# Optimization experiments

Hardware: AMD Instinct MI355X
Metric: run time of the kernel (lower is better)

## Reference

```python
import jax, jax.numpy as jnp
import numpy as np

T, B, N, DEG, F_IN, H, C = 48, 32, 96, 8, 16, 128, 500
E = B * N * DEG          # edges per timestep (already batch-offset within [0, B*N))
M = T * B * N            # total nodes across all timesteps
EPS = 1e-5               # BatchNorm eps


def setup_inputs() -> dict:
    key = jax.random.key(0)
    ks = jax.random.split(key, 24)
    rn = lambda k, s: jax.random.normal(k, s, dtype=jnp.float32) * 0.05
    return {
        "x": jax.random.normal(ks[0], (T, B * N, F_IN), dtype=jnp.float32),
        "edge_index": jax.random.randint(ks[1], (T, 2, E), 0, B * N, dtype=jnp.int32),
        "gcn_w0": rn(ks[2], (F_IN, H)),
        "gcn_w12": rn(ks[3], (2, H, H)),
        "gcn_b": rn(ks[4], (3, H)),
        "bn_gamma": jnp.ones((3, H), dtype=jnp.float32),
        "bn_beta": jnp.zeros((3, H), dtype=jnp.float32),
        "bn_mean": rn(ks[5], (3, H)),
        "bn_var": jax.random.uniform(ks[6], (3, H), minval=0.5, maxval=1.5, dtype=jnp.float32),
        "lstm_wih0": rn(ks[7], (2, 4 * H, H)),
        "lstm_whh0": rn(ks[8], (2, 4 * H, H)),
        "lstm_bih0": rn(ks[9], (2, 4 * H)),
        "lstm_bhh0": rn(ks[10], (2, 4 * H)),
        "lstm_wih1": rn(ks[11], (2, 4 * H, 2 * H)),
        "lstm_whh1": rn(ks[12], (2, 4 * H, H)),
        "lstm_bih1": rn(ks[13], (2, 4 * H)),
        "lstm_bhh1": rn(ks[14], (2, 4 * H)),
        "attn_w1": rn(ks[15], (2 * H, H)),
        "attn_b1": rn(ks[16], (H,)),
        "attn_w2": rn(ks[17], (H, 1)),
        "attn_b2": rn(ks[18], (1,)),
        "fc1_w": rn(ks[19], (2 * H, H)),
        "fc1_b": rn(ks[20], (H,)),
        "fc2_w": rn(ks[21], (H, C)),
        "fc2_b": rn(ks[22], (C,)),
    }


def _lstm_dir(x, wih, whh, bih, bhh):
    # x: [T, B, I]; PyTorch gate order i, f, g, o
    pre = jnp.einsum('tbi,gi->tbg', x, wih) + bih  # input projection hoisted out of scan
    h0 = jnp.zeros((x.shape[1], whh.shape[1]), x.dtype)

    def step(carry, p):
        h, c = carry
        g = p + h @ whh.T + bhh
        i, f, gg, o = jnp.split(g, 4, axis=-1)
        c = jax.nn.sigmoid(f) * c + jax.nn.sigmoid(i) * jnp.tanh(gg)
        h = jax.nn.sigmoid(o) * jnp.tanh(c)
        return (h, c), h

    _, hs = jax.lax.scan(step, (h0, h0), pre)
    return hs  # [T, B, Hh]


def _bilstm(x, wih, whh, bih, bhh):
    fwd = _lstm_dir(x, wih[0], whh[0], bih[0], bhh[0])
    bwd = _lstm_dir(x[::-1], wih[1], whh[1], bih[1], bhh[1])[::-1]
    return jnp.concatenate([fwd, bwd], axis=-1)  # [T, B, 2H]


def reference(x, edge_index, gcn_w0, gcn_w12, gcn_b,
              bn_gamma, bn_beta, bn_mean, bn_var,
              lstm_wih0, lstm_whh0, lstm_bih0, lstm_bhh0,
              lstm_wih1, lstm_whh1, lstm_bih1, lstm_bhh1,
              attn_w1, attn_b1, attn_w2, attn_b2,
              fc1_w, fc1_b, fc2_w, fc2_b):
    # Fold timesteps into one big node set by offsetting indices by t*B*N
    off = (jnp.arange(T, dtype=jnp.int32) * (B * N))[:, None]
    src = (edge_index[:, 0] + off).reshape(-1)
    dst = (edge_index[:, 1] + off).reshape(-1)

    # GCN symmetric norm with self-loops: deg counts incoming edges + self-loop
    deg = jax.ops.segment_sum(jnp.ones_like(src, dtype=x.dtype), dst, num_segments=M) + 1.0
    dinv = jax.lax.rsqrt(deg)
    enorm = (dinv[src] * dinv[dst])[:, None]   # per-edge norm
    self_norm = (1.0 / deg)[:, None]           # self-loop norm

    h = x.reshape(M, F_IN)
    for l in range(3):
        W = gcn_w0 if l == 0 else gcn_w12[l - 1]
        hw = h @ W  # GCNConv applies linear first
        z = jax.ops.segment_sum(hw[src] * enorm, dst, num_segments=M) + hw * self_norm + gcn_b[l]
        # BatchNorm1d eval-mode (running stats), then ReLU, residual if shapes match
        z = (z - bn_mean[l]) * (bn_gamma[l] * jax.lax.rsqrt(bn_var[l] + EPS)) + bn_beta[l]
        z = jax.nn.relu(z)
        h = z + h if l > 0 else z  # dropout is identity in eval

    # global_mean_pool per graph (fixed N nodes per graph)
    emb = h.reshape(T, B, N, H).mean(axis=2)  # [T, B, H]

    out1 = _bilstm(emb, lstm_wih0, lstm_whh0, lstm_bih0, lstm_bhh0)
    out2 = _bilstm(out1, lstm_wih1, lstm_whh1, lstm_bih1, lstm_bhh1)
    lstm_out = out2.transpose(1, 0, 2)  # [B, T, 2H]

    a = jnp.tanh(lstm_out @ attn_w1 + attn_b1) @ attn_w2 + attn_b2  # [B, T, 1]
    w = jax.nn.softmax(a, axis=1)
    ws = jnp.sum(lstm_out * w, axis=1)  # [B, 2H]

    y = jax.nn.relu(ws @ fc1_w + fc1_b) @ fc2_w + fc2_b
    return jax.nn.log_softmax(y, axis=1)
```

## Files before the change

kernel.cpp:

```cpp
#include <hip/hip_runtime.h>

#define T_ 48
#define B_ 32
#define N_ 96
#define E_ 24576
#define BN_ (B_*N_)
#define M_ (T_*BN_)
#define FIN_ 16
#define H_ 128
#define C_ 500
#define TE_ (T_*E_)
#define EPS_ 1e-5f

typedef _Float16 f16x8 __attribute__((ext_vector_type(8)));
typedef float    f32x4 __attribute__((ext_vector_type(4)));
typedef _Float16 half2v __attribute__((ext_vector_type(2)));

__device__ __forceinline__ ushort f2h(float f) {
    _Float16 h = (_Float16)f;
    union { _Float16 h; ushort u; } v;
    v.h = h;
    return v.u;
}
__device__ __forceinline__ float h2f(ushort u) {
    union { ushort u; _Float16 h; } v;
    v.u = u;
    return (float)v.h;
}
__device__ __forceinline__ half2v pkfma(unsigned int v, unsigned int w, half2v acc) {
#if __has_builtin(__builtin_elementwise_fma)
    return __builtin_elementwise_fma(__builtin_bit_cast(half2v, v),
                                     __builtin_bit_cast(half2v, w), acc);
#else
    half2v hv = __builtin_bit_cast(half2v, v);
    half2v wv = __builtin_bit_cast(half2v, w);
    acc[0] += hv[0]*wv[0];
    acc[1] += hv[1]*wv[1];
    return acc;
#endif
}
__device__ __forceinline__ float dot2pk(unsigned int hbits, unsigned int wbits, float acc) {
#if __has_builtin(__builtin_amdgcn_fdot2)
    return __builtin_amdgcn_fdot2(__builtin_bit_cast(half2v, hbits),
                                  __builtin_bit_cast(half2v, wbits), acc, false);
#else
    half2v hv = __builtin_bit_cast(half2v, hbits);
    half2v wv = __builtin_bit_cast(half2v, wbits);
    acc = fmaf((float)hv[0], (float)wv[0], acc);
    acc = fmaf((float)hv[1], (float)wv[1], acc);
    return acc;
#endif
}
__device__ __forceinline__ float sigm(float x) {
    return 1.f / (1.f + __expf(-x));
}
__device__ __forceinline__ float ftanh(float x) {
    x = fminf(15.f, fmaxf(-15.f, x));
    float e = __expf(2.f * x);
    return (e - 1.f) / (e + 1.f);
}

__global__ __launch_bounds__(1024) void csr_build_k(
    const int* __restrict__ ei, int* __restrict__ csr_off,
    unsigned int* __restrict__ csr_pk, float* __restrict__ dinv)
{
    int t = blockIdx.x;
    int tid = threadIdx.x;
    __shared__ int cnt[BN_];
    __shared__ int cur[BN_];
    __shared__ int scanbuf[1024];
    __shared__ unsigned int pk[E_];

    #pragma unroll
    for (int i = 0; i < 3; i++) cnt[tid + i*1024] = 0;
    __syncthreads();

    const int* srcp = ei + ((long)t*2+0)*E_;
    const int* dstp = ei + ((long)t*2+1)*E_;
    #pragma unroll
    for (int i = 0; i < E_/1024; i++)
        atomicAdd(&cnt[dstp[tid + i*1024]], 1);
    __syncthreads();

    int n0 = tid*3;
    int a = cnt[n0], b = cnt[n0+1], c = cnt[n0+2];
    int tot = a + b + c;
    scanbuf[tid] = tot;
    __syncthreads();
    for (int d = 1; d < 1024; d <<= 1) {
        int add = (tid >= d) ? scanbuf[tid-d] : 0;
        __syncthreads();
        scanbuf[tid] += add;
        __syncthreads();
    }
    int excl = scanbuf[tid] - tot;
    cur[n0] = excl; cur[n0+1] = excl + a; cur[n0+2] = excl + a + b;
    int gbase = t*BN_, ebase = t*E_;
    csr_off[gbase+n0]   = ebase + excl;
    csr_off[gbase+n0+1] = ebase + excl + a;
    csr_off[gbase+n0+2] = ebase + excl + a + b;
    dinv[gbase+n0]   = rsqrtf((float)a + 1.f);
    dinv[gbase+n0+1] = rsqrtf((float)b + 1.f);
    dinv[gbase+n0+2] = rsqrtf((float)c + 1.f);
    if (t == T_-1 && tid == 0) csr_off[M_] = TE_;
    __syncthreads();

    #pragma unroll
    for (int i = 0; i < E_/1024; i++) {
        int e = tid + i*1024;
        int s = srcp[e], d = dstp[e];
        int pos = atomicAdd(&cur[d], 1);
        float w = rsqrtf((float)cnt[s] + 1.f) * rsqrtf((float)cnt[d] + 1.f);
        pk[pos] = (unsigned int)s | ((unsigned int)f2h(w) << 16);
    }
    __syncthreads();

    uint4* dpk = (uint4*)(csr_pk + ebase);
    const uint4* spk = (const uint4*)pk;
    #pragma unroll
    for (int i = 0; i < E_/4096; i++)
        dpk[tid + i*1024] = spk[tid + i*1024];
}

#define WPREP_TOTAL (384+1024+4096+16384+16384+65536+65536+131072+262144)
__global__ void wprep_k(
    const float* __restrict__ gcn_b, const float* __restrict__ gam,
    const float* __restrict__ bet, const float* __restrict__ mu,
    const float* __restrict__ var,
    float* __restrict__ bn_sc, float* __restrict__ bn_sh,
    const float* __restrict__ bih0, const float* __restrict__ bhh0,
    float* __restrict__ bias0,
    const float* __restrict__ bih1, const float* __restrict__ bhh1,
    float* __restrict__ bias1,
    const float* __restrict__ gcn_w0, const float* __restrict__ gcn_w12,
    ushort* __restrict__ w0t, ushort* __restrict__ w1t, ushort* __restrict__ w2t,
    const float* __restrict__ whh0, const float* __restrict__ whh1,
    unsigned int* __restrict__ wpk0, unsigned int* __restrict__ wpk1,
    const float* __restrict__ wih0, const float* __restrict__ wih1,
    ushort* __restrict__ wih0b, ushort* __restrict__ wih1b)
{
    int i = blockIdx.x * blockDim.x + threadIdx.x;
    if (i >= WPREP_TOTAL) return;
    if (i < 384) {
        float sc = gam[i] * rsqrtf(var[i] + EPS_);
        bn_sc[i] = sc;
        bn_sh[i] = gcn_b[i]*sc + bet[i] - mu[i]*sc;
        return;
    }
    i -= 384;
    if (i < 1024) {
        bias0[i] = bih0[i] + bhh0[i];
        bias1[i] = bih1[i] + bhh1[i];
        return;
    }
    i -= 1024;
    if (i < 4096) {
        int e = i & 7, lane = (i >> 3) & 63, ct = i >> 9;
        int k = (lane >> 4)*8 + e;
        int c = ct*16 + (lane & 15);
        w0t[i] = (k < 16) ? f2h(gcn_w0[k*128 + c]) : (ushort)0;
        return;
    }
    i -= 4096;
    if (i < 16384) {
        int e = i & 7, lane = (i >> 3) & 63, kk = (i >> 9) & 3, ct = i >> 11;
        int k = kk*32 + (lane >> 4)*8 + e;
        int c = ct*16 + (lane & 15);
        w1t[i] = f2h(gcn_w12[k*128 + c]);
        return;
    }
    i -= 16384;
    if (i < 16384) {
        int e = i & 7, lane = (i >> 3) & 63, kk = (i >> 9) & 3, ct = i >> 11;
        int k = kk*32 + (lane >> 4)*8 + e;
        int c = ct*16 + (lane & 15);
        w2t[i] = f2h(gcn_w12[16384 + k*128 + c]);
        return;
    }
    i -= 16384;
    if (i < 65536) {
        int dir = i >> 15, r = i & 32767;
        int q = r >> 9, tidw = r & 511;
        int hh = tidw >> 2, gate = tidw & 3;
        int g = gate*128 + hh;
        const float* wr = whh0 + ((long)(dir*512 + g))*128 + 2*q;
        wpk0[i] = (unsigned int)f2h(wr[0]) | ((unsigned int)f2h(wr[1]) << 16);
        return;
    }
    i -= 65536;
    if (i < 65536) {
        int dir = i >> 15, r = i & 32767;
        int q = r >> 9, tidw = r & 511;
        int hh = tidw >> 2, gate = tidw & 3;
        int g = gate*128 + hh;
        const float* wr = whh1 + ((long)(dir*512 + g))*128 + 2*q;
        wpk1[i] = (unsigned int)f2h(wr[0]) | ((unsigned int)f2h(wr[1]) << 16);
        return;
    }
    i -= 65536;
    if (i < 131072) {
        int dir = i >> 16, r = i & 0xFFFF;
        int nt = r >> 11, kk = (r >> 9) & 3, lane = (r >> 3) & 63, e = r & 7;
        int n = nt*16 + (lane & 15);
        int k = kk*32 + (lane >> 4)*8 + e;
        wih0b[i] = f2h(wih0[((long)dir*512 + n)*128 + k]);
        return;
    }
    i -= 131072;
    {
        int dir = i >> 17, r = i & 0x1FFFF;
        int nt = r >> 12, kk = (r >> 9) & 7, lane = (r >> 3) & 63, e = r & 7;
        int n = nt*16 + (lane & 15);
        int k = kk*32 + (lane >> 4)*8 + e;
        wih1b[i] = f2h(wih1[((long)dir*512 + n)*256 + k]);
    }
}


__global__ __launch_bounds__(256) void gather128_k(
    const ushort* __restrict__ h, ushort* __restrict__ out,
    const int* __restrict__ csr_off, const unsigned int* __restrict__ csr_pk,
    const float* __restrict__ dinv)
{
    int nb = gridDim.x;
    int chunk = nb >> 3;
    int bswz = (blockIdx.x & 7) * chunk + (blockIdx.x >> 3);
    int wv = threadIdx.x >> 6;
    int nodeA = __builtin_amdgcn_readfirstlane(bswz*8 + wv*2);
    int tbase = (nodeA / BN_) * BN_;
    int lane = threadIdx.x & 63;
    int l2 = lane * 2;
    int e00 = __builtin_amdgcn_readfirstlane(csr_off[nodeA]);
    int e01 = __builtin_amdgcn_readfirstlane(csr_off[nodeA+1]);
    int e11 = __builtin_amdgcn_readfirstlane(csr_off[nodeA+2]);
    int dA = e01 - e00, dB = e11 - e01;
    unsigned int mypkA = (lane < dA) ? csr_pk[e00 + lane] : 0u;
    unsigned int mypkB = (lane < dB) ? csr_pk[e01 + lane] : 0u;
    float dvA = dinv[nodeA], dvB = dinv[nodeA+1];
    unsigned int selfA = *(const unsigned int*)(h + (size_t)nodeA*128 + l2);
    unsigned int selfB = *(const unsigned int*)(h + (size_t)(nodeA+1)*128 + l2);

    ushort swA = f2h(dvA * dvA), swB = f2h(dvB * dvB);
    half2v spA = __builtin_bit_cast(half2v, (unsigned int)(swA * 0x10001u));
    half2v spB = __builtin_bit_cast(half2v, (unsigned int)(swB * 0x10001u));
    half2v a0 = __builtin_bit_cast(half2v, selfA);
    a0[0] *= spA[0]; a0[1] *= spA[1];
    half2v b0 = __builtin_bit_cast(half2v, selfB);
    b0[0] *= spB[0]; b0[1] *= spB[1];
    half2v a1 = {(_Float16)0.f, (_Float16)0.f}, a2 = a1, a3 = a1;
    half2v b1 = a1, b2 = a1, b3 = a1;

    int cA = (dA < 64) ? dA : 64;
    int cB = (dB < 64) ? dB : 64;
    int cA4 = cA & ~3, cB4 = cB & ~3;
    int cm = (cA4 > cB4) ? cA4 : cB4;
    for (int j = 0; j < cm; j += 4) {
        unsigned int pA0, pA1, pA2, pA3, vA0, vA1, vA2, vA3;
        unsigned int pB0, pB1, pB2, pB3, vB0, vB1, vB2, vB3;
        bool qA = (j < cA4), qB = (j < cB4);
        if (qA) {
            pA0 = (unsigned int)__builtin_amdgcn_readlane((int)mypkA, j+0);
            pA1 = (unsigned int)__builtin_amdgcn_readlane((int)mypkA, j+1);
            pA2 = (unsigned int)__builtin_amdgcn_readlane((int)mypkA, j+2);
            pA3 = (unsigned int)__builtin_amdgcn_readlane((int)mypkA, j+3);
            vA0 = *(const unsigned int*)(h + (size_t)(tbase + (int)(pA0 & 0xffffu))*128 + l2);
            vA1 = *(const unsigned int*)(h + (size_t)(tbase + (int)(pA1 & 0xffffu))*128 + l2);
            vA2 = *(const unsigned int*)(h + (size_t)(tbase + (int)(pA2 & 0xffffu))*128 + l2);
            vA3 = *(const unsigned int*)(h + (size_t)(tbase + (int)(pA3 & 0xffffu))*128 + l2);
        }
        if (qB) {
            pB0 = (unsigned int)__builtin_amdgcn_readlane((int)mypkB, j+0);
            pB1 = (unsigned int)__builtin_amdgcn_readlane((int)mypkB, j+1);
            pB2 = (unsigned int)__builtin_amdgcn_readlane((int)mypkB, j+2);
            pB3 = (unsigned int)__builtin_amdgcn_readlane((int)mypkB, j+3);
            vB0 = *(const unsigned int*)(h + (size_t)(tbase + (int)(pB0 & 0xffffu))*128 + l2);
            vB1 = *(const unsigned int*)(h + (size_t)(tbase + (int)(pB1 & 0xffffu))*128 + l2);
            vB2 = *(const unsigned int*)(h + (size_t)(tbase + (int)(pB2 & 0xffffu))*128 + l2);
            vB3 = *(const unsigned int*)(h + (size_t)(tbase + (int)(pB3 & 0xffffu))*128 + l2);
        }
        if (qA) {
            a0 = pkfma(vA0, (pA0 >> 16) * 0x10001u, a0);
            a1 = pkfma(vA1, (pA1 >> 16) * 0x10001u, a1);
            a2 = pkfma(vA2, (pA2 >> 16) * 0x10001u, a2);
            a3 = pkfma(vA3, (pA3 >> 16) * 0x10001u, a3);
        }
        if (qB) {
            b0 = pkfma(vB0, (pB0 >> 16) * 0x10001u, b0);
            b1 = pkfma(vB1, (pB1 >> 16) * 0x10001u, b1);
            b2 = pkfma(vB2, (pB2 >> 16) * 0x10001u, b2);
            b3 = pkfma(vB3, (pB3 >> 16) * 0x10001u, b3);
        }
    }
    for (int j = cA4; j < cA; j++) {
        unsigned int pk0 = (unsigned int)__builtin_amdgcn_readlane((int)mypkA, j);
        unsigned int v = *(const unsigned int*)(h + (size_t)(tbase + (int)(pk0 & 0xffffu))*128 + l2);
        a0 = pkfma(v, (pk0 >> 16) * 0x10001u, a0);
    }
    for (int j = cB4; j < cB; j++) {
        unsigned int pk0 = (unsigned int)__builtin_amdgcn_readlane((int)mypkB, j);
        unsigned int v = *(const unsigned int*)(h + (size_t)(tbase + (int)(pk0 & 0xffffu))*128 + l2);
        b0 = pkfma(v, (pk0 >> 16) * 0x10001u, b0);
    }
    for (int jj = e00 + 64; jj < e01; jj++) {
        unsigned int pk0 = __builtin_amdgcn_readfirstlane(csr_pk[jj]);
        unsigned int v = *(const unsigned int*)(h + (size_t)(tbase + (int)(pk0 & 0xffffu))*128 + l2);
        a0 = pkfma(v, (pk0 >> 16) * 0x10001u, a0);
    }
    for (int jj = e01 + 64; jj < e11; jj++) {
        unsigned int pk0 = __builtin_amdgcn_readfirstlane(csr_pk[jj]);
        unsigned int v = *(const unsigned int*)(h + (size_t)(tbase + (int)(pk0 & 0xffffu))*128 + l2);
        b0 = pkfma(v, (pk0 >> 16) * 0x10001u, b0);
    }
    float ra0 = ((float)a0[0] + (float)a1[0]) + ((float)a2[0] + (float)a3[0]);
    float ra1 = ((float)a0[1] + (float)a1[1]) + ((float)a2[1] + (float)a3[1]);
    float rb0 = ((float)b0[0] + (float)b1[0]) + ((float)b2[0] + (float)b3[0]);
    float rb1 = ((float)b0[1] + (float)b1[1]) + ((float)b2[1] + (float)b3[1]);
    *(unsigned int*)(out + (size_t)nodeA*128 + l2) =
        (unsigned int)f2h(ra0) | ((unsigned int)f2h(ra1) << 16);
    *(unsigned int*)(out + (size_t)(nodeA+1)*128 + l2) =
        (unsigned int)f2h(rb0) | ((unsigned int)f2h(rb1) << 16);
}

__global__ __launch_bounds__(256) void gather16f_k(
    const float* __restrict__ x, ushort* __restrict__ out,
    const int* __restrict__ csr_off, const unsigned int* __restrict__ csr_pk,
    const float* __restrict__ dinv)
{
    int nb = gridDim.x;
    int chunk = nb >> 3;
    int bswz = (blockIdx.x & 7) * chunk + (blockIdx.x >> 3);
    int node = bswz * 32 + (threadIdx.x >> 3);
    int f0 = (threadIdx.x & 7) * 2;
    int tbase = (node / BN_) * BN_;
    float dv = dinv[node];
    float2 sv = *(const float2*)(x + (long)node*16 + f0);
    float s = dv * dv;
    float a0 = sv.x*s, a1 = sv.y*s;
    int e0 = csr_off[node], e1 = csr_off[node+1];
    int j = e0;
    for (; j + 4 <= e1; j += 4) {
        unsigned int p0 = csr_pk[j], p1 = csr_pk[j+1], p2 = csr_pk[j+2], p3 = csr_pk[j+3];
        int s0 = tbase + (int)(p0 & 0xffffu), s1 = tbase + (int)(p1 & 0xffffu);
        int s2 = tbase + (int)(p2 & 0xffffu), s3 = tbase + (int)(p3 & 0xffffu);
        float w0 = h2f((ushort)(p0 >> 16)), w1 = h2f((ushort)(p1 >> 16));
        float w2 = h2f((ushort)(p2 >> 16)), w3 = h2f((ushort)(p3 >> 16));
        float2 v0 = *(const float2*)(x + (long)s0*16 + f0);
        float2 v1 = *(const float2*)(x + (long)s1*16 + f0);
        float2 v2 = *(const float2*)(x + (long)s2*16 + f0);
        float2 v3 = *(const float2*)(x + (long)s3*16 + f0);
        a0 += v0.x*w0 + v1.x*w1 + v2.x*w2 + v3.x*w3;
        a1 += v0.y*w0 + v1.y*w1 + v2.y*w2 + v3.y*w3;
    }
    for (; j < e1; j++) {
        unsigned int pk = csr_pk[j];
        int sc = tbase + (int)(pk & 0xffffu);
        float en = h2f((ushort)(pk >> 16));
        float2 v = *(const float2*)(x + (long)sc*16 + f0);
        a0 += v.x*en; a1 += v.y*en;
    }
    unsigned int ov = (unsigned int)f2h(a0) | ((unsigned int)f2h(a1) << 16);
    *(unsigned int*)(out + (long)node*16 + f0) = ov;
}

template<int K, bool HASRES>
__global__ __launch_bounds__(256) void mm_mfma_k(
    const ushort* __restrict__ A, const ushort* __restrict__ Wt,
    ushort* __restrict__ Cout,
    const float* __restrict__ bnsc, const float* __restrict__ bnsh,
    const ushort* __restrict__ resid)
{
    constexpr int KST = (K >= 32) ? (K/32) : 1;
    int tid = threadIdx.x;
    int w = tid >> 6, lane = tid & 63;
    int l16 = lane & 15, lh = lane >> 4;
    int row0 = blockIdx.x * 64 + w * 16;
    __shared__ ushort cl[64][136];

    f32x4 acc[8];
    #pragma unroll
    for (int i = 0; i < 8; i++) acc[i] = (f32x4){0.f, 0.f, 0.f, 0.f};

    #pragma unroll
    for (int kk = 0; kk < KST; kk++) {
        int ka = kk*32 + lh*8;
        f16x8 af;
        bool valid = (K >= 32) || (ka < K);
        if (valid) {
            af = *reinterpret_cast<const f16x8*>(&A[(long)(row0 + l16)*K + ka]);
        } else {
            #pragma unroll
            for (int e = 0; e < 8; e++) af[e] = (_Float16)0.f;
        }
        #pragma unroll
        for (int ct = 0; ct < 8; ct++) {
            f16x8 bfr = *reinterpret_cast<const f16x8*>(
                &Wt[(((long)ct*KST + kk)*64 + lane)*8]);
            acc[ct] = __builtin_amdgcn_mfma_f32_16x16x32_f16(af, bfr, acc[ct], 0, 0, 0);
        }
    }

    #pragma unroll
    for (int ct = 0; ct < 8; ct++) {
        int col = ct*16 + l16;
        float sc = bnsc[col], sh = bnsh[col];
        #pragma unroll
        for (int r = 0; r < 4; r++) {
            int rl = w*16 + lh*4 + r;
            float v = acc[ct][r] * sc + sh;
            cl[rl][col] = f2h(fmaxf(v, 0.f));
        }
    }
    __syncthreads();
    long rowblock = (long)blockIdx.x * 64;
    #pragma unroll
    for (int it = 0; it < 4; it++) {
        int s = it*256 + tid;
        int rl = s >> 4, c8 = (s & 15) * 8;
        uint4 v = *(const uint4*)&cl[rl][c8];
        if (HASRES) {
            uint4 rv = *(const uint4*)&resid[(rowblock + rl)*128 + c8];
            half2v* vv = (half2v*)&v;
            const half2v* rr = (const half2v*)&rv;
            vv[0] += rr[0]; vv[1] += rr[1]; vv[2] += rr[2]; vv[3] += rr[3];
        }
        *(uint4*)&Cout[(rowblock + rl)*128 + c8] = v;
    }
}

template<int K>
__global__ __launch_bounds__(256) void mm_pre_k(
    const ushort* __restrict__ A, const ushort* __restrict__ Wt_all,
    float* __restrict__ Cout_all, const float* __restrict__ bias_all)
{
    constexpr int KST = K/32;
    int dir = blockIdx.z;
    const ushort* Wt = Wt_all + (size_t)dir * 512 * K;
    float* Cout = Cout_all + (size_t)dir * T_ * B_ * 512;
    const float* bias = bias_all + dir * 512;

    int tid = threadIdx.x;
    int w = tid >> 6, lane = tid & 63;
    int l16 = lane & 15, lh = lane >> 4;
    int row0 = blockIdx.x * 64 + w * 16;
    int nt0 = blockIdx.y * 8;

    f32x4 acc[8];
    #pragma unroll
    for (int i = 0; i < 8; i++) acc[i] = (f32x4){0.f, 0.f, 0.f, 0.f};

    #pragma unroll
    for (int kk = 0; kk < KST; kk++) {
        int ka = kk*32 + lh*8;
        f16x8 af = *reinterpret_cast<const f16x8*>(&A[(long)(row0 + l16)*K + ka]);
        #pragma unroll
        for (int ct = 0; ct < 8; ct++) {
            f16x8 bfr = *reinterpret_cast<const f16x8*>(
                &Wt[(((long)(nt0 + ct)*KST + kk)*64 + lane)*8]);
            acc[ct] = __builtin_amdgcn_mfma_f32_16x16x32_f16(af, bfr, acc[ct], 0, 0, 0);
        }
    }

    #pragma unroll
    for (int ct = 0; ct < 8; ct++) {
        int col = (nt0 + ct)*16 + l16;
        float bv = bias[col];
        int colp = ((col & 127) << 2) | (col >> 7);
        #pragma unroll
        for (int r = 0; r < 4; r++) {
            int row = row0 + lh*4 + r;
            Cout[(long)row*512 + colp] = acc[ct][r] + bv;
        }
    }
}


__global__ void meanpool_k(const ushort* __restrict__ h, ushort* __restrict__ embb) {
    int row = blockIdx.x;
    int t = row / B_, b = row - t*B_;
    int hh = threadIdx.x;
    const ushort* base = h + ((long)t*BN_ + b*N_)*H_ + hh;
    float acc = 0.f;
    for (int n = 0; n < N_; n++) acc += h2f(base[(long)n*H_]);
    embb[(long)row*H_ + hh] = f2h(acc * (1.f / N_));
}

__global__ __launch_bounds__(512) void lstm_scan_k(
    const float* __restrict__ pre,
    const unsigned int* __restrict__ wpkbuf,
    float* __restrict__ out,
    ushort* __restrict__ outb)
{
    int dir = blockIdx.x >> 5;
    int b   = blockIdx.x & 31;
    int tid = threadIdx.x;
    int lane = tid & 63;
    int laneBase = lane & ~3;
    int hh = tid >> 2;

    __shared__ ushort hbuf[2][H_];
    if (tid < 2*H_) ((ushort*)hbuf)[tid] = 0;
    float creg = 0.f;

    const unsigned int* wp = wpkbuf + (long)dir * 64 * 512;
    unsigned int wpk[64];
    #pragma unroll
    for (int q = 0; q < 64; q++) wpk[q] = wp[q*512 + tid];

    const float* pred = pre + (long)dir * T_ * B_ * 512;
    int t = dir ? (T_ - 1) : 0;
    int tstep = dir ? -1 : 1;
    float pv = pred[((long)t*B_ + b)*512 + tid];
    __syncthreads();

    for (int st = 0; st < T_; st++) {
        int tn = t + tstep;
        tn = (tn < 0) ? 0 : ((tn >= T_) ? T_ - 1 : tn);
        float pvn = pred[((long)tn*B_ + b)*512 + tid];

        const uint4* h4 = (const uint4*)hbuf[st & 1];
        float a0 = pv, a1 = 0.f, a2 = 0.f, a3 = 0.f;
        #pragma unroll
        for (int jj = 0; jj < 16; jj++) {
            uint4 hv = h4[jj];
            a0 = dot2pk(hv.x, wpk[jj*4+0], a0);
            a1 = dot2pk(hv.y, wpk[jj*4+1], a1);
            a2 = dot2pk(hv.z, wpk[jj*4+2], a2);
            a3 = dot2pk(hv.w, wpk[jj*4+3], a3);
        }
        float sum = (a0 + a1) + (a2 + a3);

        float ig = __shfl(sum, laneBase + 0, 64);
        float fg = __shfl(sum, laneBase + 1, 64);
        float gg = __shfl(sum, laneBase + 2, 64);
        float og = __shfl(sum, laneBase + 3, 64);
        float c = sigm(fg) * creg + sigm(ig) * ftanh(gg);
        float h = sigm(og) * ftanh(c);
        creg = c;
        if ((tid & 3) == 0) {
            hbuf[(st + 1) & 1][hh] = f2h(h);
            long orow = ((long)t*B_ + b)*256 + dir*H_ + hh;
            if (out)  out[orow] = h;
            if (outb) outb[orow] = f2h(h);
        }
        __syncthreads();
        pv = pvn;
        t = tn;
    }
}


__global__ __launch_bounds__(128) void attn_a_k(
    const float* __restrict__ out2, const float* __restrict__ w1,
    const float* __restrict__ b1, const float* __restrict__ w2,
    const float* __restrict__ b2v, float* __restrict__ a)
{
    int row = blockIdx.x;
    int j = threadIdx.x;
    const float* xr = out2 + (long)row * 256;
    float acc = b1[j];
    for (int k = 0; k < 256; k++) acc += xr[k] * w1[k*128 + j];
    float u = tanhf(acc) * w2[j];
    __shared__ float red[128];
    red[j] = u;
    __syncthreads();
    for (int d = 64; d > 0; d >>= 1) {
        if (j < d) red[j] += red[j + d];
        __syncthreads();
    }
    if (j == 0) {
        int t = row / B_, b = row - t*B_;
        a[b*T_ + t] = red[0] + b2v[0];
    }
}

__global__ __launch_bounds__(256) void attn_pool_k(
    const float* __restrict__ out2, const float* __restrict__ a,
    float* __restrict__ wsv)
{
    int b = blockIdx.x;
    __shared__ float w[T_];
    if (threadIdx.x == 0) {
        float m = -1e30f;
        for (int t = 0; t < T_; t++) m = fmaxf(m, a[b*T_ + t]);
        float s = 0.f;
        for (int t = 0; t < T_; t++) { float e = __expf(a[b*T_ + t] - m); w[t] = e; s += e; }
        float inv = 1.f / s;
        for (int t = 0; t < T_; t++) w[t] *= inv;
    }
    __syncthreads();
    int h2 = threadIdx.x;
    float acc = 0.f;
    for (int t = 0; t < T_; t++) acc += w[t] * out2[((long)t*B_ + b)*256 + h2];
    wsv[b*256 + h2] = acc;
}


__global__ __launch_bounds__(512) void head_k(
    const float* __restrict__ wsv, const float* __restrict__ w1,
    const float* __restrict__ b1, const float* __restrict__ w2,
    const float* __restrict__ b2, float* __restrict__ outp)
{
    int b = blockIdx.x;
    int tid = threadIdx.x;
    __shared__ float r[128];
    __shared__ float y[C_];
    __shared__ float red[512];
    if (tid < 128) {
        float acc = b1[tid];
        for (int k = 0; k < 256; k++) acc += wsv[b*256 + k] * w1[k*128 + tid];
        r[tid] = fmaxf(acc, 0.f);
    }
    __syncthreads();
    for (int c = tid; c < C_; c += 512) {
        float acc = b2[c];
        for (int k = 0; k < 128; k++) acc += r[k] * w2[k*C_ + c];
        y[c] = acc;
    }
    __syncthreads();
    float m = -1e30f;
    for (int c = tid; c < C_; c += 512) m = fmaxf(m, y[c]);
    red[tid] = m;
    __syncthreads();
    for (int d = 256; d > 0; d >>= 1) {
        if (tid < d) red[tid] = fmaxf(red[tid], red[tid + d]);
        __syncthreads();
    }
    m = red[0];
    __syncthreads();
    float s = 0.f;
    for (int c = tid; c < C_; c += 512) s += __expf(y[c] - m);
    red[tid] = s;
    __syncthreads();
    for (int d = 256; d > 0; d >>= 1) {
        if (tid < d) red[tid] += red[tid + d];
        __syncthreads();
    }
    float lse = m + logf(red[0]);
    for (int c = tid; c < C_; c += 512) outp[(long)b*C_ + c] = y[c] - lse;
}


extern "C" void kernel_launch(void* const* d_in, const int* in_sizes, int n_in,
                              void* d_out, int out_size, void* d_ws, size_t ws_size,
                              hipStream_t stream) {
    const float* x        = (const float*)d_in[0];
    const int*   ei       = (const int*)d_in[1];
    const float* gcn_w0   = (const float*)d_in[2];
    const float* gcn_w12  = (const float*)d_in[3];
    const float* gcn_b    = (const float*)d_in[4];
    const float* bn_gamma = (const float*)d_in[5];
    const float* bn_beta  = (const float*)d_in[6];
    const float* bn_mean  = (const float*)d_in[7];
    const float* bn_var   = (const float*)d_in[8];
    const float* wih0     = (const float*)d_in[9];
    const float* whh0     = (const float*)d_in[10];
    const float* bih0     = (const float*)d_in[11];
    const float* bhh0     = (const float*)d_in[12];
    const float* wih1     = (const float*)d_in[13];
    const float* whh1     = (const float*)d_in[14];
    const float* bih1     = (const float*)d_in[15];
    const float* bhh1     = (const float*)d_in[16];
    const float* attn_w1  = (const float*)d_in[17];
    const float* attn_b1  = (const float*)d_in[18];
    const float* attn_w2  = (const float*)d_in[19];
    const float* attn_b2  = (const float*)d_in[20];
    const float* fc1_w    = (const float*)d_in[21];
    const float* fc1_b    = (const float*)d_in[22];
    const float* fc2_w    = (const float*)d_in[23];
    const float* fc2_b    = (const float*)d_in[24];

    char* p = (char*)d_ws;
    auto alloc = [&](size_t bytes) {
        void* r = (void*)p;
        p += (bytes + 255) & ~(size_t)255;
        return r;
    };
    ushort* aggbuf = (ushort*)alloc((size_t)M_*H_*2);
    ushort* hbA    = (ushort*)alloc((size_t)M_*H_*2);
    ushort* hbB    = (ushort*)alloc((size_t)M_*H_*2);
    float* dinv    = (float*)alloc((size_t)M_*4);
    int*   csr_off = (int*)  alloc((size_t)(M_+1)*4);
    unsigned int* csr_pk = (unsigned int*)alloc((size_t)TE_*4);
    float* bn_sc   = (float*)alloc(384*4);
    float* bn_sh   = (float*)alloc(384*4);
    float* bias0   = (float*)alloc(1024*4);
    float* bias1   = (float*)alloc(1024*4);
    ushort* w0t    = (ushort*)alloc((size_t)4096*2);
    ushort* w1t    = (ushort*)alloc((size_t)16384*2);
    ushort* w2t    = (ushort*)alloc((size_t)16384*2);
    unsigned int* wpk0 = (unsigned int*)alloc((size_t)2*64*512*4);
    unsigned int* wpk1 = (unsigned int*)alloc((size_t)2*64*512*4);
    ushort* wih0b  = (ushort*)alloc((size_t)2*512*128*2);
    ushort* wih1b  = (ushort*)alloc((size_t)2*512*256*2);
    ushort* embb   = (ushort*)alloc((size_t)T_*B_*H_*2);
    float* pre     = (float*)alloc((size_t)2*T_*B_*512*4);
    ushort* out1b  = (ushort*)alloc((size_t)T_*B_*256*2);
    float* out2v   = (float*)alloc((size_t)T_*B_*256*4);
    float* attn_av = (float*)alloc((size_t)B_*T_*4);
    float* wsv     = (float*)alloc((size_t)B_*256*4);

    csr_build_k<<<T_, 1024, 0, stream>>>(ei, csr_off, csr_pk, dinv);

    wprep_k<<<(WPREP_TOTAL+255)/256, 256, 0, stream>>>(
        gcn_b, bn_gamma, bn_beta, bn_mean, bn_var, bn_sc, bn_sh,
        bih0, bhh0, bias0, bih1, bhh1, bias1,
        gcn_w0, gcn_w12, w0t, w1t, w2t,
        whh0, whh1, wpk0, wpk1,
        wih0, wih1, wih0b, wih1b);

    gather16f_k<<<M_/32, 256, 0, stream>>>(x, aggbuf, csr_off, csr_pk, dinv);
    mm_mfma_k<16, false><<<M_/64, 256, 0, stream>>>(aggbuf, w0t, hbA,
                                                    bn_sc + 0, bn_sh + 0, nullptr);
    gather128_k<<<M_/8, 256, 0, stream>>>(hbA, aggbuf, csr_off, csr_pk, dinv);
    mm_mfma_k<128, true><<<M_/64, 256, 0, stream>>>(aggbuf, w1t, hbB,
                                                    bn_sc + 128, bn_sh + 128, hbA);
    gather128_k<<<M_/8, 256, 0, stream>>>(hbB, aggbuf, csr_off, csr_pk, dinv);
    mm_mfma_k<128, true><<<M_/64, 256, 0, stream>>>(aggbuf, w2t, hbA,
                                                    bn_sc + 256, bn_sh + 256, hbB);

    meanpool_k<<<T_*B_, 128, 0, stream>>>(hbA, embb);

    mm_pre_k<128><<<dim3((T_*B_)/64, 4, 2), 256, 0, stream>>>(embb, wih0b, pre, bias0);
    lstm_scan_k<<<64, 512, 0, stream>>>(pre, wpk0, nullptr, out1b);

    mm_pre_k<256><<<dim3((T_*B_)/64, 4, 2), 256, 0, stream>>>(out1b, wih1b, pre, bias1);
    lstm_scan_k<<<64, 512, 0, stream>>>(pre, wpk1, out2v, nullptr);

    attn_a_k<<<T_*B_, 128, 0, stream>>>(out2v, attn_w1, attn_b1, attn_w2, attn_b2, attn_av);
    attn_pool_k<<<B_, 256, 0, stream>>>(out2v, attn_av, wsv);

    head_k<<<B_, 512, 0, stream>>>(wsv, fc1_w, fc1_b, fc2_w, fc2_b, (float*)d_out);
}
```

Baseline: 323.1 us.

## Halve LSTM scan block size with two gates per thread

The recurrent LSTM scan now uses 256 threads per block instead of 512. Each thread computes two gate dot products (128 packed weight registers), and one xor shuffle exchanges partial gates between thread pairs instead of four shuffles within quads. The weight packing and the pre-activation column permutation are rearranged to match the new thread-to-gate mapping. This cuts the number of waves taking part in each per-step barrier and raises per-thread ILP, at the cost of doubled register pressure for the weights.

```diff
diff --git a/kernel.cpp b/kernel.cpp
--- a/kernel.cpp
+++ b/kernel.cpp
@@ -180,9 +180,10 @@
     i -= 16384;
     if (i < 65536) {
         int dir = i >> 15, r = i & 32767;
-        int q = r >> 9, tidw = r & 511;
-        int hh = tidw >> 2, gate = tidw & 3;
-        int g = gate*128 + hh;
+        int ab = r >> 14, r2 = r & 16383;
+        int q = r2 >> 8, tidw = r2 & 255;
+        int hh = tidw >> 1, gp = tidw & 1;
+        int g = (2*gp + ab)*128 + hh;
         const float* wr = whh0 + ((long)(dir*512 + g))*128 + 2*q;
         wpk0[i] = (unsigned int)f2h(wr[0]) | ((unsigned int)f2h(wr[1]) << 16);
         return;
@@ -190,9 +191,10 @@
     i -= 65536;
     if (i < 65536) {
         int dir = i >> 15, r = i & 32767;
-        int q = r >> 9, tidw = r & 511;
-        int hh = tidw >> 2, gate = tidw & 3;
-        int g = gate*128 + hh;
+        int ab = r >> 14, r2 = r & 16383;
+        int q = r2 >> 8, tidw = r2 & 255;
+        int hh = tidw >> 1, gp = tidw & 1;
+        int g = (2*gp + ab)*128 + hh;
         const float* wr = whh1 + ((long)(dir*512 + g))*128 + 2*q;
         wpk1[i] = (unsigned int)f2h(wr[0]) | ((unsigned int)f2h(wr[1]) << 16);
         return;
@@ -464,7 +466,8 @@
     for (int ct = 0; ct < 8; ct++) {
         int col = (nt0 + ct)*16 + l16;
         float bv = bias[col];
-        int colp = ((col & 127) << 2) | (col >> 7);
+        int gate = col >> 7, hh = col & 127;
+        int colp = (gate & 1)*256 + hh*2 + (gate >> 1);
         #pragma unroll
         for (int r = 0; r < 4; r++) {
             int row = row0 + lh*4 + r;
@@ -484,7 +487,7 @@
     embb[(long)row*H_ + hh] = f2h(acc * (1.f / N_));
 }
 
-__global__ __launch_bounds__(512) void lstm_scan_k(
+__global__ __launch_bounds__(256) void lstm_scan_k(
     const float* __restrict__ pre,
     const unsigned int* __restrict__ wpkbuf,
     float* __restrict__ out,
@@ -493,57 +496,69 @@
     int dir = blockIdx.x >> 5;
     int b   = blockIdx.x & 31;
     int tid = threadIdx.x;
-    int lane = tid & 63;
-    int laneBase = lane & ~3;
-    int hh = tid >> 2;
+    int gp  = tid & 1;
+    int hh  = tid >> 1;
 
     __shared__ ushort hbuf[2][H_];
-    if (tid < 2*H_) ((ushort*)hbuf)[tid] = 0;
+    ((ushort*)hbuf)[tid] = 0;
     float creg = 0.f;
 
-    const unsigned int* wp = wpkbuf + (long)dir * 64 * 512;
-    unsigned int wpk[64];
-    #pragma unroll
-    for (int q = 0; q < 64; q++) wpk[q] = wp[q*512 + tid];
+    const unsigned int* wpA = wpkbuf + ((long)dir*2 + 0)*64*256;
+    const unsigned int* wpB = wpkbuf + ((long)dir*2 + 1)*64*256;
+    unsigned int wA[64], wB[64];
+    #pragma unroll
+    for (int q = 0; q < 64; q++) {
+        wA[q] = wpA[q*256 + tid];
+        wB[q] = wpB[q*256 + tid];
+    }
 
     const float* pred = pre + (long)dir * T_ * B_ * 512;
     int t = dir ? (T_ - 1) : 0;
     int tstep = dir ? -1 : 1;
-    float pv = pred[((long)t*B_ + b)*512 + tid];
+    float pvA = pred[(((long)t*B_ + b)*2 + 0)*256 + tid];
+    float pvB = pred[(((long)t*B_ + b)*2 + 1)*256 + tid];
     __syncthreads();
 
     for (int st = 0; st < T_; st++) {
         int tn = t + tstep;
         tn = (tn < 0) ? 0 : ((tn >= T_) ? T_ - 1 : tn);
-        float pvn = pred[((long)tn*B_ + b)*512 + tid];
+        float pvAn = pred[(((long)tn*B_ + b)*2 + 0)*256 + tid];
+        float pvBn = pred[(((long)tn*B_ + b)*2 + 1)*256 + tid];
 
         const uint4* h4 = (const uint4*)hbuf[st & 1];
-        float a0 = pv, a1 = 0.f, a2 = 0.f, a3 = 0.f;
+        float a0 = pvA, a1 = 0.f, a2 = 0.f, a3 = 0.f;
+        float c0 = pvB, c1 = 0.f, c2 = 0.f, c3 = 0.f;
         #pragma unroll
         for (int jj = 0; jj < 16; jj++) {
             uint4 hv = h4[jj];
-            a0 = dot2pk(hv.x, wpk[jj*4+0], a0);
-            a1 = dot2pk(hv.y, wpk[jj*4+1], a1);
-            a2 = dot2pk(hv.z, wpk[jj*4+2], a2);
-            a3 = dot2pk(hv.w, wpk[jj*4+3], a3);
-        }
-        float sum = (a0 + a1) + (a2 + a3);
-
-        float ig = __shfl(sum, laneBase + 0, 64);
-        float fg = __shfl(sum, laneBase + 1, 64);
-        float gg = __shfl(sum, laneBase + 2, 64);
-        float og = __shfl(sum, laneBase + 3, 64);
+            a0 = dot2pk(hv.x, wA[jj*4+0], a0);
+            a1 = dot2pk(hv.y, wA[jj*4+1], a1);
+            a2 = dot2pk(hv.z, wA[jj*4+2], a2);
+            a3 = dot2pk(hv.w, wA[jj*4+3], a3);
+            c0 = dot2pk(hv.x, wB[jj*4+0], c0);
+            c1 = dot2pk(hv.y, wB[jj*4+1], c1);
+            c2 = dot2pk(hv.z, wB[jj*4+2], c2);
+            c3 = dot2pk(hv.w, wB[jj*4+3], c3);
+        }
+        float sA = (a0 + a1) + (a2 + a3);
+        float sB = (c0 + c1) + (c2 + c3);
+        float oA = __shfl_xor(sA, 1, 64);
+        float oB = __shfl_xor(sB, 1, 64);
+        float ig = gp ? oA : sA;
+        float fg = gp ? oB : sB;
+        float gg = gp ? sA : oA;
+        float og = gp ? sB : oB;
         float c = sigm(fg) * creg + sigm(ig) * ftanh(gg);
         float h = sigm(og) * ftanh(c);
         creg = c;
-        if ((tid & 3) == 0) {
+        if (gp == 0) {
             hbuf[(st + 1) & 1][hh] = f2h(h);
             long orow = ((long)t*B_ + b)*256 + dir*H_ + hh;
             if (out)  out[orow] = h;
             if (outb) outb[orow] = f2h(h);
         }
         __syncthreads();
-        pv = pvn;
+        pvA = pvAn; pvB = pvBn;
         t = tn;
     }
 }
@@ -721,10 +736,10 @@
     meanpool_k<<<T_*B_, 128, 0, stream>>>(hbA, embb);
 
     mm_pre_k<128><<<dim3((T_*B_)/64, 4, 2), 256, 0, stream>>>(embb, wih0b, pre, bias0);
-    lstm_scan_k<<<64, 512, 0, stream>>>(pre, wpk0, nullptr, out1b);
+    lstm_scan_k<<<64, 256, 0, stream>>>(pre, wpk0, nullptr, out1b);
 
     mm_pre_k<256><<<dim3((T_*B_)/64, 4, 2), 256, 0, stream>>>(out1b, wih1b, pre, bias1);
-    lstm_scan_k<<<64, 512, 0, stream>>>(pre, wpk1, out2v, nullptr);
+    lstm_scan_k<<<64, 256, 0, stream>>>(pre, wpk1, out2v, nullptr);
 
     attn_a_k<<<T_*B_, 128, 0, stream>>>(out2v, attn_w1, attn_b1, attn_w2, attn_b2, attn_av);
     attn_pool_k<<<B_, 256, 0, stream>>>(out2v, attn_av, wsv);
```

New measurement: 314.3 us. 1.03x faster.
